# Kernel tuning notes

Hardware: AMD Instinct MI355X
Metric: run time of the kernel (lower is better)

Reference implementation:

```python
import jax, jax.numpy as jnp
import numpy as np

HEAD_SIZE = 64
NUM_HEADS = 16
D_MODEL = HEAD_SIZE * NUM_HEADS
BATCH = 2
SEQ = 2048


def setup_inputs() -> dict:
    key = jax.random.key(0)
    ks = jax.random.split(key, 9)
    s = 1.0 / np.sqrt(D_MODEL)
    inp = {
        "hidden_states": jax.random.normal(ks[0], (BATCH, SEQ, D_MODEL), jnp.float32),
        "Wq": jax.random.uniform(ks[1], (D_MODEL, D_MODEL), jnp.float32, -s, s),
        "bq": jax.random.uniform(ks[2], (D_MODEL,), jnp.float32, -s, s),
        "Wk": jax.random.uniform(ks[3], (D_MODEL, D_MODEL), jnp.float32, -s, s),
        "bk": jax.random.uniform(ks[4], (D_MODEL,), jnp.float32, -s, s),
        "Wv": jax.random.uniform(ks[5], (D_MODEL, D_MODEL), jnp.float32, -s, s),
        "bv": jax.random.uniform(ks[6], (D_MODEL,), jnp.float32, -s, s),
        "Wo": jax.random.uniform(ks[7], (D_MODEL, D_MODEL), jnp.float32, -s, s),
        "bo": jax.random.uniform(ks[8], (D_MODEL,), jnp.float32, -s, s),
    }
    return inp


def _split_heads(x):
    # [B, S, H*D] -> [B, H, S, D]
    b, s, _ = x.shape
    return x.reshape(b, s, NUM_HEADS, HEAD_SIZE).transpose(0, 2, 1, 3)


def reference(hidden_states, Wq, bq, Wk, bk, Wv, bv, Wo, bo):
    q = _split_heads(hidden_states @ Wq + bq)  # [B,H,S,D]
    k = _split_heads(hidden_states @ Wk + bk)
    v = _split_heads(hidden_states @ Wv + bv)
    scale = 1.0 / jnp.sqrt(jnp.asarray(HEAD_SIZE, hidden_states.dtype))
    scores = jnp.einsum("bhqd,bhkd->bhqk", q, k) * scale  # [B,H,S,S]
    weights = jax.nn.softmax(scores, axis=-1)
    attended = jnp.einsum("bhqk,bhkd->bhqd", weights, v)  # [B,H,S,D]
    merged = attended.transpose(0, 2, 1, 3).reshape(hidden_states.shape)  # [B,S,H*D]
    return merged @ Wo + bo
```

## Files before the change

kernel.cpp:

```cpp
#include <hip/hip_runtime.h>
#include <hip/hip_bf16.h>

#define D_MODEL 1024
#define HEADS 16
#define HSZ 64
#define BATCH 2
#define SEQ 2048
#define TOK (BATCH*SEQ)
#define NT (SEQ/64)

typedef __attribute__((ext_vector_type(8))) short bf16x8;
typedef __attribute__((ext_vector_type(4))) float f32x4;

#define QSCALE 0.1803368801111244f
#define THR_L2 11.541560327f

static __device__ __forceinline__ unsigned short f2bf(float f) {
  union { float f; unsigned u; } v; v.f = f;
  unsigned r = v.u + 0x7fffu + ((v.u >> 16) & 1u);
  return (unsigned short)(r >> 16);
}

static __device__ __forceinline__ float exp2_fast(float x) {
  float r;
  asm("v_exp_f32 %0, %1" : "=v"(r) : "v"(x));
  return r;
}

static __device__ __forceinline__ unsigned cvt_pk_bf16(float a, float b) {
  unsigned r;
  asm("v_cvt_pk_bf16_f32 %0, %1, %2" : "=v"(r) : "v"(a), "v"(b));
  return r;
}

static __device__ __forceinline__ int swz128(int row, int g) {
  return ((row << 7) + (g << 4)) ^ ((row & 7) << 4);
}

static __device__ __forceinline__ int xs4(int lr) {
  return ((lr & 7) << 1) | (lr >> 3);
}

static __device__ __forceinline__ void load_lds16(const void* g, void* l) {
  __builtin_amdgcn_global_load_lds(
      (const __attribute__((address_space(1))) unsigned*)g,
      (__attribute__((address_space(3))) unsigned*)l, 16, 0, 0);
}


__global__ void cvt_bf16_kernel(const float* __restrict__ src,
                                unsigned short* __restrict__ dst, int n) {
  int i = (blockIdx.x * blockDim.x + threadIdx.x) * 8;
  if (i >= n) return;
  float4 v0 = *reinterpret_cast<const float4*>(src + i);
  float4 v1 = *reinterpret_cast<const float4*>(src + i + 4);
  ushort4 o0, o1;
  o0.x = f2bf(v0.x); o0.y = f2bf(v0.y); o0.z = f2bf(v0.z); o0.w = f2bf(v0.w);
  o1.x = f2bf(v1.x); o1.y = f2bf(v1.y); o1.z = f2bf(v1.z); o1.w = f2bf(v1.w);
  *reinterpret_cast<ushort4*>(dst + i) = o0;
  *reinterpret_cast<ushort4*>(dst + i + 4) = o1;
}

__global__ void transpose_cvt_kernel(const float* __restrict__ Wq, const float* __restrict__ Wk,
                                     const float* __restrict__ Wv, const float* __restrict__ Wo,
                                     unsigned short* __restrict__ Wqkvt,
                                     unsigned short* __restrict__ Wot) {
  __shared__ float tile[32][33];
  int m = blockIdx.z;
  const float* src = (m == 0) ? Wq : (m == 1) ? Wk : (m == 2) ? Wv : Wo;
  unsigned short* dst = (m < 3) ? (Wqkvt + (size_t)m * D_MODEL * D_MODEL) : Wot;
  int i0 = blockIdx.y * 32, o0 = blockIdx.x * 32;
  int tx = threadIdx.x, ty = threadIdx.y;
  for (int k = 0; k < 32; k += 8)
    tile[ty + k][tx] = src[(size_t)(i0 + ty + k) * D_MODEL + o0 + tx];
  __syncthreads();
  for (int k = 0; k < 32; k += 8)
    dst[(size_t)(o0 + ty + k) * D_MODEL + i0 + tx] = f2bf(tile[tx][ty + k]);
}


template<int EPI>
__global__ __launch_bounds__(256) void gemm128_kernel(
    const unsigned short* __restrict__ A, const unsigned short* __restrict__ Bt,
    int K, int N,
    const float* __restrict__ b0, const float* __restrict__ b1, const float* __restrict__ b2,
    unsigned short* __restrict__ Qb, unsigned short* __restrict__ Kb,
    unsigned short* __restrict__ Vtb, float* __restrict__ Cout)
{
  __shared__ char As[128 * 64];
  __shared__ char Bs[128 * 64];
  int m0 = blockIdx.y * 128, n0 = blockIdx.x * 128;
  int tid = threadIdx.x;
  int wv = tid >> 6, l = tid & 63;
  int wm = wv >> 1, wn = wv & 1;
  int lg = l >> 4, lr = l & 15;
  int srow = wv * 32 + (l >> 2);
  int scol = (l & 3) * 8;

  f32x4 acc[4][4];
#pragma unroll
  for (int i = 0; i < 4; i++)
#pragma unroll
    for (int j = 0; j < 4; j++) acc[i][j] = (f32x4){0.f, 0.f, 0.f, 0.f};

  for (int k0 = 0; k0 < K; k0 += 32) {
    __syncthreads();
    const unsigned short* ga = A  + (size_t)(m0 + srow) * K + k0 + scol;
    const unsigned short* gb = Bt + (size_t)(n0 + srow) * K + k0 + scol;
    load_lds16(ga,                       As + wv * 2048);
    load_lds16(ga + (size_t)16 * K,      As + wv * 2048 + 1024);
    load_lds16(gb,                       Bs + wv * 2048);
    load_lds16(gb + (size_t)16 * K,      Bs + wv * 2048 + 1024);
    __syncthreads();

    bf16x8 af[4], bfv[4];
#pragma unroll
    for (int mi = 0; mi < 4; mi++)
      af[mi] = *reinterpret_cast<const bf16x8*>(As + (wm * 64 + mi * 16 + lr) * 64 + lg * 16);
#pragma unroll
    for (int ni = 0; ni < 4; ni++)
      bfv[ni] = *reinterpret_cast<const bf16x8*>(Bs + (wn * 64 + ni * 16 + lr) * 64 + lg * 16);
#pragma unroll
    for (int mi = 0; mi < 4; mi++)
#pragma unroll
      for (int ni = 0; ni < 4; ni++)
        acc[mi][ni] = __builtin_amdgcn_mfma_f32_16x16x32_bf16(af[mi], bfv[ni], acc[mi][ni], 0, 0, 0);
  }

#pragma unroll
  for (int mi = 0; mi < 4; mi++) {
    int gr0 = m0 + wm * 64 + mi * 16 + lg * 4;
#pragma unroll
    for (int ni = 0; ni < 4; ni++) {
      int gc = n0 + wn * 64 + ni * 16 + lr;
      if (EPI == 0) {
        int mat = gc >> 10, o = gc & 1023;
        int hh = o >> 6, d = o & 63;
        const float* bias = (mat == 0) ? b0 : (mat == 1) ? b1 : b2;
        float bv = bias[o];
#pragma unroll
        for (int r = 0; r < 4; r++) {
          int t = gr0 + r;
          int b = t >> 11, s = t & 2047;
          float v = acc[mi][ni][r] + bv;
          if (mat == 0) v *= QSCALE;
          unsigned short u = f2bf(v);
          size_t head = (size_t)(b * HEADS + hh);
          if (mat == 0)      Qb [(head * SEQ + s) * HSZ + d] = u;
          else if (mat == 1) Kb [(head * SEQ + s) * HSZ + d] = u;
          else               Vtb[(head * HSZ + d) * SEQ + s] = u;
        }
      } else {
        float bv = b0[gc];
#pragma unroll
        for (int r = 0; r < 4; r++) {
          int t = gr0 + r;
          Cout[(size_t)t * N + gc] = acc[mi][ni][r] + bv;
        }
      }
    }
  }
}


__global__ __launch_bounds__(512, 4) void attn_kernel(
    const unsigned short* __restrict__ Qb, const unsigned short* __restrict__ Kb,
    const unsigned short* __restrict__ Vtb, unsigned short* __restrict__ Mg)
{
  __shared__ char Ks[64 * 128];
  __shared__ char Vs[64 * 128];
  __shared__ char Ps[8][16 * 128];

  int orig = blockIdx.y * 16 + blockIdx.x;
  int swzb = (orig & 7) * 64 + (orig >> 3);
  int bh = swzb >> 4;
  int q0 = (swzb & 15) * 128;
  int b = bh >> 4, h = bh & 15;
  int tid = threadIdx.x, w = tid >> 6, l = tid & 63;
  int lg = l >> 4, lr = l & 15;
  const unsigned short* Qh = Qb + (size_t)bh * SEQ * HSZ;
  const unsigned short* Kh = Kb + (size_t)bh * SEQ * HSZ;
  const unsigned short* Vh = Vtb + (size_t)bh * HSZ * SEQ;

  bf16x8 qf2[2];
#pragma unroll
  for (int k2 = 0; k2 < 2; k2++)
    qf2[k2] = *reinterpret_cast<const bf16x8*>(
        Qh + (size_t)(q0 + w * 16 + lr) * HSZ + k2 * 32 + lg * 8);

  f32x4 of[4];
  f32x4 lones;
#pragma unroll
  for (int ni = 0; ni < 4; ni++) of[ni] = (f32x4){0.f, 0.f, 0.f, 0.f};
  lones = (f32x4){0.f, 0.f, 0.f, 0.f};
  float m_r = -1e30f;

  bf16x8 vone;
#pragma unroll
  for (int j = 0; j < 8; j++) vone[j] = (short)0x3F80;

  int srow = tid >> 3, sg = tid & 7;

  uint4 ka = *reinterpret_cast<const uint4*>(Kh + (size_t)srow * HSZ + sg * 8);
  uint4 va = *reinterpret_cast<const uint4*>(Vh + (size_t)srow * SEQ + sg * 8);

  for (int kt = 0; kt < NT; ++kt) {
    __syncthreads();
    *reinterpret_cast<uint4*>(Ks + swz128(srow, sg)) = ka;
    *reinterpret_cast<uint4*>(Vs + swz128(srow, sg)) = va;
    __syncthreads();

    if (kt + 1 < NT) {
      ka = *reinterpret_cast<const uint4*>(Kh + (size_t)((kt + 1) * 64 + srow) * HSZ + sg * 8);
      va = *reinterpret_cast<const uint4*>(Vh + (size_t)srow * SEQ + (kt + 1) * 64 + sg * 8);
    }

    f32x4 sf[4];
#pragma unroll
    for (int ni = 0; ni < 4; ni++) {
      sf[ni] = (f32x4){0.f, 0.f, 0.f, 0.f};
#pragma unroll
      for (int k2 = 0; k2 < 2; k2++) {
        bf16x8 kf = *reinterpret_cast<const bf16x8*>(Ks + swz128(ni * 16 + lr, k2 * 4 + lg));
        sf[ni] = __builtin_amdgcn_mfma_f32_16x16x32_bf16(kf, qf2[k2], sf[ni], 0, 0, 0);
      }
    }

    float lm = fmaxf(fmaxf(fmaxf(sf[0][0], sf[0][1]), fmaxf(sf[0][2], sf[0][3])),
                     fmaxf(fmaxf(sf[1][0], sf[1][1]), fmaxf(sf[1][2], sf[1][3])));
    lm = fmaxf(lm,
         fmaxf(fmaxf(fmaxf(sf[2][0], sf[2][1]), fmaxf(sf[2][2], sf[2][3])),
               fmaxf(fmaxf(sf[3][0], sf[3][1]), fmaxf(sf[3][2], sf[3][3]))));

    if (__any(lm > m_r + THR_L2)) {
      float vm = fmaxf(lm, __shfl_xor(lm, 16));
      vm = fmaxf(vm, __shfl_xor(vm, 32));
      float mn = fmaxf(m_r, vm);
      float al = exp2_fast(m_r - mn);
      m_r = mn;
#pragma unroll
      for (int r = 0; r < 4; r++) {
        float a = __shfl(al, lg * 4 + r, 16);
        lones[r] *= a;
#pragma unroll
        for (int ni = 0; ni < 4; ni++) of[ni][r] *= a;
      }
    }

#pragma unroll
    for (int ni = 0; ni < 4; ni++) {
      float p0 = exp2_fast(sf[ni][0] - m_r);
      float p1 = exp2_fast(sf[ni][1] - m_r);
      float p2 = exp2_fast(sf[ni][2] - m_r);
      float p3 = exp2_fast(sf[ni][3] - m_r);
      uint2 pw;
      pw.x = cvt_pk_bf16(p0, p1);
      pw.y = cvt_pk_bf16(p2, p3);
      int slot = (ni * 4 + lg) ^ xs4(lr);
      *reinterpret_cast<uint2*>(Ps[w] + (lr << 7) + (slot << 3)) = pw;
    }

    bf16x8 pa[2];
#pragma unroll
    for (int k2 = 0; k2 < 2; k2++) {
      int g0 = k2 * 8 + lg * 2;
      uint2 lo = *reinterpret_cast<const uint2*>(Ps[w] + (lr << 7) + (((g0)     ^ xs4(lr)) << 3));
      uint2 hi = *reinterpret_cast<const uint2*>(Ps[w] + (lr << 7) + (((g0 + 1) ^ xs4(lr)) << 3));
      int4 t = {(int)lo.x, (int)lo.y, (int)hi.x, (int)hi.y};
      pa[k2] = *reinterpret_cast<bf16x8*>(&t);
    }

    __builtin_amdgcn_s_setprio(1);
#pragma unroll
    for (int k2 = 0; k2 < 2; k2++)
      lones = __builtin_amdgcn_mfma_f32_16x16x32_bf16(pa[k2], vone, lones, 0, 0, 0);
#pragma unroll
    for (int ni = 0; ni < 4; ni++)
#pragma unroll
      for (int k2 = 0; k2 < 2; k2++) {
        bf16x8 vf = *reinterpret_cast<const bf16x8*>(Vs + swz128(ni * 16 + lr, k2 * 4 + lg));
        of[ni] = __builtin_amdgcn_mfma_f32_16x16x32_bf16(pa[k2], vf, of[ni], 0, 0, 0);
      }
    __builtin_amdgcn_s_setprio(0);
  }

#pragma unroll
  for (int r = 0; r < 4; r++) {
    float inv = 1.0f / lones[r];
    int q = q0 + w * 16 + lg * 4 + r;
#pragma unroll
    for (int ni = 0; ni < 4; ni++) {
      int dm = h * 64 + ni * 16 + lr;
      Mg[(size_t)(b * SEQ + q) * D_MODEL + dm] = f2bf(of[ni][r] * inv);
    }
  }
}


extern "C" void kernel_launch(void* const* d_in, const int* in_sizes, int n_in,
                              void* d_out, int out_size, void* d_ws, size_t ws_size,
                              hipStream_t stream) {
  const float* X  = (const float*)d_in[0];
  const float* Wq = (const float*)d_in[1];
  const float* bq = (const float*)d_in[2];
  const float* Wk = (const float*)d_in[3];
  const float* bk = (const float*)d_in[4];
  const float* Wv = (const float*)d_in[5];
  const float* bv = (const float*)d_in[6];
  const float* Wo = (const float*)d_in[7];
  const float* bo = (const float*)d_in[8];
  float* out = (float*)d_out;

  char* ws = (char*)d_ws;
  unsigned short* Xbf   = (unsigned short*)(ws);
  unsigned short* Wqkvt = (unsigned short*)(ws + ((size_t)8  << 20));
  unsigned short* Wot   = (unsigned short*)(ws + ((size_t)14 << 20));
  unsigned short* Qb    = (unsigned short*)(ws + ((size_t)16 << 20));
  unsigned short* Kb    = (unsigned short*)(ws + ((size_t)24 << 20));
  unsigned short* Vtb   = (unsigned short*)(ws + ((size_t)32 << 20));
  unsigned short* Mg = Xbf;

  cvt_bf16_kernel<<<(TOK * D_MODEL / 8 + 255) / 256, 256, 0, stream>>>(X, Xbf, TOK * D_MODEL);
  transpose_cvt_kernel<<<dim3(32, 32, 4), dim3(32, 8), 0, stream>>>(Wq, Wk, Wv, Wo, Wqkvt, Wot);
  gemm128_kernel<0><<<dim3(24, 32), 256, 0, stream>>>(Xbf, Wqkvt, 1024, 3072,
                                                      bq, bk, bv, Qb, Kb, Vtb, nullptr);
  attn_kernel<<<dim3(16, 32), 512, 0, stream>>>(Qb, Kb, Vtb, Mg);
  gemm128_kernel<1><<<dim3(8, 32), 256, 0, stream>>>(Mg, Wot, 1024, 1024,
                                                     bo, nullptr, nullptr,
                                                     nullptr, nullptr, nullptr, out);
}
```

Before: 209.0 us.

## Double-buffer attention K/V tiles via direct global-to-LDS loads, pre-swizzled in GEMM

```diff
diff --git a/kernel.cpp b/kernel.cpp
--- a/kernel.cpp
+++ b/kernel.cpp
@@ -89,7 +89,11 @@
 {
   __shared__ char As[128 * 64];
   __shared__ char Bs[128 * 64];
-  int m0 = blockIdx.y * 128, n0 = blockIdx.x * 128;
+  int gx = gridDim.x;
+  int orig = blockIdx.y * gx + blockIdx.x;
+  int chunk = (gx * gridDim.y) >> 3;
+  int sw = (orig & 7) * chunk + (orig >> 3);
+  int m0 = (sw / gx) * 128, n0 = (sw % gx) * 128;
   int tid = threadIdx.x;
   int wv = tid >> 6, l = tid & 63;
   int wm = wv >> 1, wn = wv & 1;
@@ -146,9 +150,12 @@
           if (mat == 0) v *= QSCALE;
           unsigned short u = f2bf(v);
           size_t head = (size_t)(b * HEADS + hh);
-          if (mat == 0)      Qb [(head * SEQ + s) * HSZ + d] = u;
-          else if (mat == 1) Kb [(head * SEQ + s) * HSZ + d] = u;
-          else               Vtb[(head * HSZ + d) * SEQ + s] = u;
+          if (mat == 0)
+            Qb[(head * SEQ + s) * HSZ + d] = u;
+          else if (mat == 1)
+            Kb[((head * SEQ + s) * HSZ + d) ^ ((s & 7) << 3)] = u;
+          else
+            Vtb[(((head * HSZ + d) * SEQ + s)) ^ ((d & 7) << 3)] = u;
         }
       } else {
         float bv = b0[gc];
@@ -163,13 +170,15 @@
 }
 
 
+#define KOFF(c) ((c) * 8192)
+#define VOFF(c) (16384 + (c) * 8192)
+#define POFF(w) (32768 + (w) * 2048)
+
 __global__ __launch_bounds__(512, 4) void attn_kernel(
     const unsigned short* __restrict__ Qb, const unsigned short* __restrict__ Kb,
     const unsigned short* __restrict__ Vtb, unsigned short* __restrict__ Mg)
 {
-  __shared__ char Ks[64 * 128];
-  __shared__ char Vs[64 * 128];
-  __shared__ char Ps[8][16 * 128];
+  __shared__ char lds[49152];
 
   int orig = blockIdx.y * 16 + blockIdx.x;
   int swzb = (orig & 7) * 64 + (orig >> 3);
@@ -179,8 +188,20 @@
   int tid = threadIdx.x, w = tid >> 6, l = tid & 63;
   int lg = l >> 4, lr = l & 15;
   const unsigned short* Qh = Qb + (size_t)bh * SEQ * HSZ;
-  const unsigned short* Kh = Kb + (size_t)bh * SEQ * HSZ;
-  const unsigned short* Vh = Vtb + (size_t)bh * HSZ * SEQ;
+  const char* Kg = (const char*)(Kb + (size_t)bh * SEQ * HSZ) + (size_t)tid * 16;
+  const char* Vg = (const char*)(Vtb + (size_t)bh * HSZ * SEQ)
+                   + (size_t)(tid >> 3) * (SEQ * 2) + (tid & 7) * 16;
+
+  int dsb[2] = { swz128(lr, lg), swz128(lr, lg + 4) };
+  int pwa[4], paa[4];
+#pragma unroll
+  for (int ni = 0; ni < 4; ni++)
+    pwa[ni] = POFF(w) + (lr << 7) + ((((ni << 2) + lg) ^ xs4(lr)) << 3);
+#pragma unroll
+  for (int k2 = 0; k2 < 2; k2++)
+#pragma unroll
+    for (int hh = 0; hh < 2; hh++)
+      paa[k2 * 2 + hh] = POFF(w) + (lr << 7) + (((k2 * 8 + lg * 2 + hh) ^ xs4(lr)) << 3);
 
   bf16x8 qf2[2];
 #pragma unroll
@@ -189,31 +210,24 @@
         Qh + (size_t)(q0 + w * 16 + lr) * HSZ + k2 * 32 + lg * 8);
 
   f32x4 of[4];
-  f32x4 lones;
+  f32x4 lones = (f32x4){0.f, 0.f, 0.f, 0.f};
 #pragma unroll
   for (int ni = 0; ni < 4; ni++) of[ni] = (f32x4){0.f, 0.f, 0.f, 0.f};
-  lones = (f32x4){0.f, 0.f, 0.f, 0.f};
   float m_r = -1e30f;
 
   bf16x8 vone;
 #pragma unroll
   for (int j = 0; j < 8; j++) vone[j] = (short)0x3F80;
 
-  int srow = tid >> 3, sg = tid & 7;
-
-  uint4 ka = *reinterpret_cast<const uint4*>(Kh + (size_t)srow * HSZ + sg * 8);
-  uint4 va = *reinterpret_cast<const uint4*>(Vh + (size_t)srow * SEQ + sg * 8);
-
-  for (int kt = 0; kt < NT; ++kt) {
-    __syncthreads();
-    *reinterpret_cast<uint4*>(Ks + swz128(srow, sg)) = ka;
-    *reinterpret_cast<uint4*>(Vs + swz128(srow, sg)) = va;
-    __syncthreads();
-
-    if (kt + 1 < NT) {
-      ka = *reinterpret_cast<const uint4*>(Kh + (size_t)((kt + 1) * 64 + srow) * HSZ + sg * 8);
-      va = *reinterpret_cast<const uint4*>(Vh + (size_t)srow * SEQ + (kt + 1) * 64 + sg * 8);
-    }
+  auto stage = [&](int t, int nb) {
+    if (t < NT) {
+      load_lds16(Kg + (size_t)t * 8192, lds + KOFF(nb) + w * 1024);
+      load_lds16(Vg + (size_t)t * 128,  lds + VOFF(nb) + w * 1024);
+    }
+  };
+
+  auto body = [&](int t, int cur) {
+    stage(t + 1, cur ^ 1);
 
     f32x4 sf[4];
 #pragma unroll
@@ -221,7 +235,7 @@
       sf[ni] = (f32x4){0.f, 0.f, 0.f, 0.f};
 #pragma unroll
       for (int k2 = 0; k2 < 2; k2++) {
-        bf16x8 kf = *reinterpret_cast<const bf16x8*>(Ks + swz128(ni * 16 + lr, k2 * 4 + lg));
+        bf16x8 kf = *reinterpret_cast<const bf16x8*>(lds + dsb[k2] + KOFF(cur) + ni * 2048);
         sf[ni] = __builtin_amdgcn_mfma_f32_16x16x32_bf16(kf, qf2[k2], sf[ni], 0, 0, 0);
       }
     }
@@ -249,25 +263,19 @@
 
 #pragma unroll
     for (int ni = 0; ni < 4; ni++) {
-      float p0 = exp2_fast(sf[ni][0] - m_r);
-      float p1 = exp2_fast(sf[ni][1] - m_r);
-      float p2 = exp2_fast(sf[ni][2] - m_r);
-      float p3 = exp2_fast(sf[ni][3] - m_r);
       uint2 pw;
-      pw.x = cvt_pk_bf16(p0, p1);
-      pw.y = cvt_pk_bf16(p2, p3);
-      int slot = (ni * 4 + lg) ^ xs4(lr);
-      *reinterpret_cast<uint2*>(Ps[w] + (lr << 7) + (slot << 3)) = pw;
+      pw.x = cvt_pk_bf16(exp2_fast(sf[ni][0] - m_r), exp2_fast(sf[ni][1] - m_r));
+      pw.y = cvt_pk_bf16(exp2_fast(sf[ni][2] - m_r), exp2_fast(sf[ni][3] - m_r));
+      *reinterpret_cast<uint2*>(lds + pwa[ni]) = pw;
     }
 
     bf16x8 pa[2];
 #pragma unroll
     for (int k2 = 0; k2 < 2; k2++) {
-      int g0 = k2 * 8 + lg * 2;
-      uint2 lo = *reinterpret_cast<const uint2*>(Ps[w] + (lr << 7) + (((g0)     ^ xs4(lr)) << 3));
-      uint2 hi = *reinterpret_cast<const uint2*>(Ps[w] + (lr << 7) + (((g0 + 1) ^ xs4(lr)) << 3));
-      int4 t = {(int)lo.x, (int)lo.y, (int)hi.x, (int)hi.y};
-      pa[k2] = *reinterpret_cast<bf16x8*>(&t);
+      uint2 lo = *reinterpret_cast<const uint2*>(lds + paa[k2 * 2]);
+      uint2 hi = *reinterpret_cast<const uint2*>(lds + paa[k2 * 2 + 1]);
+      int4 tt = {(int)lo.x, (int)lo.y, (int)hi.x, (int)hi.y};
+      pa[k2] = *reinterpret_cast<bf16x8*>(&tt);
     }
 
     __builtin_amdgcn_s_setprio(1);
@@ -278,10 +286,19 @@
     for (int ni = 0; ni < 4; ni++)
 #pragma unroll
       for (int k2 = 0; k2 < 2; k2++) {
-        bf16x8 vf = *reinterpret_cast<const bf16x8*>(Vs + swz128(ni * 16 + lr, k2 * 4 + lg));
+        bf16x8 vf = *reinterpret_cast<const bf16x8*>(lds + dsb[k2] + VOFF(cur) + ni * 2048);
         of[ni] = __builtin_amdgcn_mfma_f32_16x16x32_bf16(pa[k2], vf, of[ni], 0, 0, 0);
       }
     __builtin_amdgcn_s_setprio(0);
+
+    __syncthreads();
+  };
+
+  stage(0, 0);
+  __syncthreads();
+  for (int kt = 0; kt < NT; kt += 2) {
+    body(kt, 0);
+    body(kt + 1, 1);
   }
 
 #pragma unroll
```

New measurement: 203.7 us. 2.6% less time.
